# Kernel optimization log

Hardware: AMD Instinct MI355X
Metric: run time of the kernel (lower is better)

The kernel has to match this reference:

```python
import jax, jax.numpy as jnp
import numpy as np

N, E, C, FIN, FOUT = 4096, 5, 2, 128, 64
DENSITY = 0.01


def setup_inputs() -> dict:
    key = jax.random.key(0)
    ks = jax.random.split(key, 8)
    vals = jax.random.uniform(ks[0], (E, N, N), dtype=jnp.float32)
    mask = jax.random.uniform(ks[1], (E, N, N)) < DENSITY
    A = jnp.where(mask, vals, 0.0)                      # [E,N,N] edge-type adjacencies (A[e,u,v]: u->v)
    h = jax.random.normal(ks[2], (N, FIN), dtype=jnp.float32)
    W1_0 = 0.01 * jax.random.normal(ks[3], (C, E), dtype=jnp.float32)  # GTConv init: normal(std=0.01)
    W2_0 = 0.01 * jax.random.normal(ks[4], (C, E), dtype=jnp.float32)
    W1_1 = 0.01 * jax.random.normal(ks[5], (C, E), dtype=jnp.float32)
    gcn_W = jax.random.normal(ks[6], (C, FIN, FOUT), dtype=jnp.float32) / np.sqrt(FIN)
    gcn_b = jnp.zeros((C, FOUT), dtype=jnp.float32)
    return {"A": A, "h": h, "W1_0": W1_0, "W2_0": W2_0, "W1_1": W1_1,
            "gcn_W": gcn_W, "gcn_b": gcn_b}


def reference(A, h, W1_0, W2_0, W1_1, gcn_W, gcn_b):
    # Structural support of the summed graphs (union of edge-type edges).
    mask = (A != 0).any(axis=0)                         # [N,N]

    def gtconv(filt):
        # weighted sum of edge-type adjacencies per channel: dgl.adj_sum_graph
        return jnp.einsum('ce,euv->cuv', filt, A)       # [C,N,N]

    def right_norm(M, sum_axis):
        # EdgeWeightNorm(norm='right'): divide each edge weight by total in-weight at dst
        d = M.sum(axis=sum_axis, keepdims=True)
        return M / jnp.where(d != 0, d, 1.0)

    def softmax_norm(S):
        # exp on existing edges only, then right-normalize over in-edges (src axis=1)
        w = jnp.where(mask, jnp.exp(S), 0.0)
        return right_norm(w, sum_axis=1)

    # Layer 0 (first=True)
    RA = softmax_norm(gtconv(W1_0))                     # first_adj, [C,N,N]
    RB = softmax_norm(gtconv(W2_0))
    H0 = jnp.einsum('cuk,ckv->cuv', RA, RB)             # dgl.adj_product_graph
    # Layer 1 (first=False): result_A = H0, result_B = conv1(A) (no softmax)
    RB1 = gtconv(W1_1)
    H1 = jnp.einsum('cuk,ckv->cuv', H0, RB1)

    layers = jnp.stack([RA, H0, H1], axis=1)            # [C,3,N,N] = layer_list per channel
    Wn = right_norm(layers, sum_axis=2)                 # right norm over src (axis u)
    # GraphConv(norm='none', activation=relu) with edge_weight: out[v] = relu(sum_u w[u,v] h[u] W + b)
    agg = jnp.einsum('cluv,uf->clvf', Wn, h)            # [C,3,N,FIN]
    out = jax.nn.relu(jnp.einsum('clvf,cfo->clvo', agg, gcn_W) + gcn_b[:, None, None, :])
    return out                                          # [C,3,N,FOUT]
```

## Files before the change

### kernel.cpp

```cpp
#include <hip/hip_runtime.h>
#include <hip/hip_bf16.h>

#define NN    4096
#define NE    5
#define NC    2
#define FINF  128
#define FOUTF 64
#define CAP   384
#define YP    132
#define VB    16


__global__ __launch_bounds__(256) void zero_cnt(int4* __restrict__ cnt4)
{
    cnt4[blockIdx.x * 256 + threadIdx.x] = int4{0, 0, 0, 0};
}

__global__ __launch_bounds__(256) void build_csc(
    const float* __restrict__ A,
    const float* __restrict__ W1_0,
    const float* __restrict__ W2_0,
    const float* __restrict__ W1_1,
    int*    __restrict__ cnt,
    int*    __restrict__ eu,
    float2* __restrict__ wA,
    float2* __restrict__ wB,
    float2* __restrict__ wC)
{
    float fA0[NE], fA1[NE], fB0[NE], fB1[NE], fC0[NE], fC1[NE];
#pragma unroll
    for (int e = 0; e < NE; ++e) {
        fA0[e] = W1_0[e];      fA1[e] = W1_0[NE + e];
        fB0[e] = W2_0[e];      fB1[e] = W2_0[NE + e];
        fC0[e] = W1_1[e];      fC1[e] = W1_1[NE + e];
    }

    const size_t S = (size_t)NN * NN / 4;
    const float4* A4 = (const float4*)A;
    size_t stride = (size_t)gridDim.x * blockDim.x;
    for (size_t i = (size_t)blockIdx.x * blockDim.x + threadIdx.x; i < S; i += stride) {
        float4 q0 = A4[i];
        float4 q1 = A4[i + S];
        float4 q2 = A4[i + 2 * S];
        float4 q3 = A4[i + 3 * S];
        float4 q4 = A4[i + 4 * S];
        int u  = (int)(i >> 10);
        int v0 = ((int)i & 1023) << 2;
#define DO_COMP(comp, joff)                                                      \
        {                                                                        \
            float a0 = q0.comp, a1 = q1.comp, a2 = q2.comp,                      \
                  a3 = q3.comp, a4 = q4.comp;                                    \
            if (a0 != 0.f || a1 != 0.f || a2 != 0.f || a3 != 0.f || a4 != 0.f) { \
                float sA0 = fA0[0]*a0 + fA0[1]*a1 + fA0[2]*a2 + fA0[3]*a3 + fA0[4]*a4; \
                float sA1 = fA1[0]*a0 + fA1[1]*a1 + fA1[2]*a2 + fA1[3]*a3 + fA1[4]*a4; \
                float sB0 = fB0[0]*a0 + fB0[1]*a1 + fB0[2]*a2 + fB0[3]*a3 + fB0[4]*a4; \
                float sB1 = fB1[0]*a0 + fB1[1]*a1 + fB1[2]*a2 + fB1[3]*a3 + fB1[4]*a4; \
                float sC0 = fC0[0]*a0 + fC0[1]*a1 + fC0[2]*a2 + fC0[3]*a3 + fC0[4]*a4; \
                float sC1 = fC1[0]*a0 + fC1[1]*a1 + fC1[2]*a2 + fC1[3]*a3 + fC1[4]*a4; \
                int v = v0 + joff;                                               \
                int pos = atomicAdd(&cnt[v], 1);                                 \
                if (pos < CAP) {                                                 \
                    int slot = v * CAP + pos;                                    \
                    eu[slot] = u;                                                \
                    wA[slot] = float2{__expf(sA0), __expf(sA1)};                 \
                    wB[slot] = float2{__expf(sB0), __expf(sB1)};                 \
                    wC[slot] = float2{sC0, sC1};                                 \
                }                                                                \
            }                                                                    \
        }
        DO_COMP(x, 0)
        DO_COMP(y, 1)
        DO_COMP(z, 2)
        DO_COMP(w, 3)
#undef DO_COMP
    }
}

template<int STAGE>
__global__ __launch_bounds__(256) void spmm_col(
    const int*    __restrict__ cnt,
    const int*    __restrict__ eu,
    const float2* __restrict__ ew,
    const float*  __restrict__ Xf,
    const ushort* __restrict__ Xb_in,
    const float*  __restrict__ Dd_in,
    float*        __restrict__ Y,
    ushort*       __restrict__ Xb_out,
    float*        __restrict__ Dd_out)
{
    int v = blockIdx.x;
    int n = cnt[v];
    if (n > CAP) n = CAP;

    __shared__ float4 s_e[CAP];
    __shared__ float  s_red[4];
    __shared__ float4 s_acc[NC][8][32];

    int tid = threadIdx.x;
    if (tid < 4) s_red[tid] = 0.f;
    __syncthreads();

    float l0 = 0.f, l1 = 0.f, ld0 = 0.f, ld1 = 0.f;
    for (int i = tid; i < n; i += 256) {
        int    u = eu[v * CAP + i];
        float2 w = ew[v * CAP + i];
        s_e[i] = float4{__int_as_float(u), w.x, w.y, 0.f};
        l0 += w.x;
        l1 += w.y;
        if (STAGE != 0) {
            ld0 += w.x * Dd_in[u];
            ld1 += w.y * Dd_in[NN + u];
        }
    }
    if (STAGE == 0) { ld0 = l0; ld1 = l1; }

#pragma unroll
    for (int m = 32; m >= 1; m >>= 1) {
        l0  += __shfl_xor(l0,  m);
        l1  += __shfl_xor(l1,  m);
        ld0 += __shfl_xor(ld0, m);
        ld1 += __shfl_xor(ld1, m);
    }
    if ((tid & 63) == 0) {
        atomicAdd(&s_red[0], l0);
        atomicAdd(&s_red[1], l1);
        atomicAdd(&s_red[2], ld0);
        atomicAdd(&s_red[3], ld1);
    }
    __syncthreads();

    int grp = tid >> 5, lane = tid & 31;
    float4 a0 = {0.f, 0.f, 0.f, 0.f};
    float4 a1 = {0.f, 0.f, 0.f, 0.f};

    if (STAGE == 0) {
        const float4* X4 = (const float4*)Xf;
        for (int i = grp; i < n; i += 8) {
            float4 e = s_e[i];
            float4 x = X4[(size_t)__float_as_int(e.x) * 32 + lane];
            a0.x += e.y * x.x; a0.y += e.y * x.y; a0.z += e.y * x.z; a0.w += e.y * x.w;
            a1.x += e.z * x.x; a1.y += e.z * x.y; a1.z += e.z * x.z; a1.w += e.z * x.w;
        }
    } else {
        const uint2* P0 = (const uint2*)Xb_in;
        const uint2* P1 = P0 + (size_t)NN * 32;
        for (int i = grp; i < n; i += 8) {
            float4 e = s_e[i];
            int u = __float_as_int(e.x);
            uint2 b0 = P0[(size_t)u * 32 + lane];
            uint2 b1 = P1[(size_t)u * 32 + lane];
            a0.x += e.y * __uint_as_float(b0.x << 16);
            a0.y += e.y * __uint_as_float(b0.x & 0xffff0000u);
            a0.z += e.y * __uint_as_float(b0.y << 16);
            a0.w += e.y * __uint_as_float(b0.y & 0xffff0000u);
            a1.x += e.z * __uint_as_float(b1.x << 16);
            a1.y += e.z * __uint_as_float(b1.x & 0xffff0000u);
            a1.z += e.z * __uint_as_float(b1.y << 16);
            a1.w += e.z * __uint_as_float(b1.y & 0xffff0000u);
        }
    }

    s_acc[0][grp][lane] = a0;
    s_acc[1][grp][lane] = a1;
    __syncthreads();

    int c = tid >> 7, f = tid & 127;
    const float* base = (const float*)s_acc[c];
    float s = 0.f;
#pragma unroll
    for (int g = 0; g < 8; ++g) s += base[g * 128 + f];

    float inv = 1.f;
    if (STAGE < 2 && n > 0) inv = 1.f / s_red[c];
    float val = s * inv;

    float* yrow = Y + ((size_t)c * NN + v) * YP;
    yrow[f] = val;
    if (STAGE < 2) {
        __hip_bfloat16 hb = __float2bfloat16(val);
        Xb_out[((size_t)c * NN + v) * FINF + f] = *(const ushort*)&hb;
    }
    if (f == 0) {
        float dvn = s_red[2 + c] * inv;
        yrow[FINF] = dvn;
        if (STAGE < 2) Dd_out[c * NN + v] = dvn;
    }
}

__global__ __launch_bounds__(64) void gcn_out(
    const float* __restrict__ YA,
    const float* __restrict__ Y1,
    const float* __restrict__ Y2,
    const float* __restrict__ gW,
    const float* __restrict__ gb,
    float* __restrict__ out)
{
    const int grids_per_cl = NN / VB;
    int b   = blockIdx.x;
    int grp = b / grids_per_cl;
    int v0  = (b % grids_per_cl) * VB;
    int c = grp / 3, l = grp % 3;
    const float* Y = (l == 0) ? YA : (l == 1) ? Y1 : Y2;

    __shared__ float s_y[VB][FINF];
    __shared__ float s_inv[VB];
    int t = threadIdx.x;

    for (int k = t; k < VB * (FINF / 4); k += 64) {
        int r = k >> 5, c4 = k & 31;
        float4 q = *(const float4*)(Y + ((size_t)c * NN + v0 + r) * YP + c4 * 4);
        *(float4*)&s_y[r][c4 * 4] = q;
    }
    if (t < VB) {
        float d = Y[((size_t)c * NN + v0 + t) * YP + FINF];
        s_inv[t] = (d != 0.f) ? (1.f / d) : 1.f;
    }
    __syncthreads();

    float acc[VB];
#pragma unroll
    for (int r = 0; r < VB; ++r) acc[r] = 0.f;

    const float* w = gW + (size_t)c * FINF * FOUTF + t;
    for (int f4 = 0; f4 < FINF / 4; ++f4) {
        float w0 = w[(size_t)(f4 * 4 + 0) * FOUTF];
        float w1 = w[(size_t)(f4 * 4 + 1) * FOUTF];
        float w2 = w[(size_t)(f4 * 4 + 2) * FOUTF];
        float w3 = w[(size_t)(f4 * 4 + 3) * FOUTF];
#pragma unroll
        for (int r = 0; r < VB; ++r) {
            float4 y4 = *(const float4*)&s_y[r][f4 * 4];
            acc[r] += y4.x * w0 + y4.y * w1 + y4.z * w2 + y4.w * w3;
        }
    }

    float bias = gb[c * FOUTF + t];
#pragma unroll
    for (int r = 0; r < VB; ++r) {
        float val = acc[r] * s_inv[r] + bias;
        out[((size_t)grp * NN + v0 + r) * FOUTF + t] = fmaxf(val, 0.f);
    }
}

extern "C" void kernel_launch(void* const* d_in, const int* in_sizes, int n_in,
                              void* d_out, int out_size, void* d_ws, size_t ws_size,
                              hipStream_t stream)
{
    const float* A     = (const float*)d_in[0];
    const float* h     = (const float*)d_in[1];
    const float* W1_0  = (const float*)d_in[2];
    const float* W2_0  = (const float*)d_in[3];
    const float* W1_1  = (const float*)d_in[4];
    const float* gW    = (const float*)d_in[5];
    const float* gb    = (const float*)d_in[6];
    float* out = (float*)d_out;

    char* ws = (char*)d_ws;
    int*    cnt = (int*)(ws);
    int*    eu  = (int*)(ws + 16384);
    float2* wA  = (float2*)(ws + 6307840);
    float2* wB  = (float2*)(ws + 18890752);
    float2* wC  = (float2*)(ws + 31473664);
    float*  YA  = (float*)(ws + 44056576);
    float*  Y1  = (float*)(ws + 48381952);
    float*  Y2  = (float*)(ws + 52707328);
    float*  DdA = (float*)(ws + 57032704);
    float*  Dd1 = (float*)(ws + 57065472);
    ushort* XbA = (ushort*)(ws + 57098240);
    ushort* Xb1 = (ushort*)(ws + 59195392);

    zero_cnt<<<4, 256, 0, stream>>>((int4*)cnt);
    build_csc<<<2048, 256, 0, stream>>>(A, W1_0, W2_0, W1_1, cnt, eu, wA, wB, wC);

    spmm_col<0><<<NN, 256, 0, stream>>>(cnt, eu, wA, h, nullptr, nullptr, YA, XbA, DdA);
    spmm_col<1><<<NN, 256, 0, stream>>>(cnt, eu, wB, nullptr, XbA, DdA, Y1, Xb1, Dd1);
    spmm_col<2><<<NN, 256, 0, stream>>>(cnt, eu, wC, nullptr, Xb1, Dd1, Y2, nullptr, nullptr);

    gcn_out<<<6 * NN / VB, 64, 0, stream>>>(YA, Y1, Y2, gW, gb, out);
}
```

Measured before the change: 227.3 us.

## Tile CSC build by column block with LDS counters and bf16 feature input

The CSC build now gives each block a 16-column by 1024-row tile of A. Per-column counts are kept in shared-memory atomics and written into per-segment slots, which removes the global atomic contention and the separate zero-count kernel. The sparse aggregation reads the four segment counts and compacts them into shared memory. The first-stage input h is converted to bf16 by a new small kernel, which halves its gather traffic at some cost in precision. The gather loops are also unrolled by two. The tiled reads of A are less sequential than the old grid-stride stream, and the per-segment cap can drop edges if a quarter-column holds more than 128 nonzeros.

```diff
diff --git a/kernel.cpp b/kernel.cpp
--- a/kernel.cpp
+++ b/kernel.cpp
@@ -1,19 +1,33 @@
 #include <hip/hip_runtime.h>
 #include <hip/hip_bf16.h>
 
-#define NN    4096
-#define NE    5
-#define NC    2
-#define FINF  128
-#define FOUTF 64
-#define CAP   384
-#define YP    132
-#define VB    16
-
-
-__global__ __launch_bounds__(256) void zero_cnt(int4* __restrict__ cnt4)
-{
-    cnt4[blockIdx.x * 256 + threadIdx.x] = int4{0, 0, 0, 0};
+#define NN     4096
+#define NE     5
+#define NC     2
+#define FINF   128
+#define FOUTF  64
+#define CAP    512
+#define SEGCAP 128
+#define USPLIT 4
+#define YP     132
+#define VB     16
+
+
+static __device__ __forceinline__ unsigned bf16bits(float x)
+{
+    __hip_bfloat16 t = __float2bfloat16(x);
+    return (unsigned)*reinterpret_cast<unsigned short*>(&t);
+}
+
+__global__ __launch_bounds__(256) void h2b(const float4* __restrict__ h4,
+                                           uint2* __restrict__ hb)
+{
+    int i = blockIdx.x * 256 + threadIdx.x;
+    float4 f = h4[i];
+    uint2 r;
+    r.x = bf16bits(f.x) | (bf16bits(f.y) << 16);
+    r.y = bf16bits(f.z) | (bf16bits(f.w) << 16);
+    hb[i] = r;
 }
 
 __global__ __launch_bounds__(256) void build_csc(
@@ -21,12 +35,22 @@
     const float* __restrict__ W1_0,
     const float* __restrict__ W2_0,
     const float* __restrict__ W1_1,
-    int*    __restrict__ cnt,
+    int*    __restrict__ cnt2,
     int*    __restrict__ eu,
     float2* __restrict__ wA,
     float2* __restrict__ wB,
     float2* __restrict__ wC)
 {
+    __shared__ int lcnt[16];
+    int tid = threadIdx.x;
+    if (tid < 16) lcnt[tid] = 0;
+    __syncthreads();
+
+    int vb = blockIdx.x & 255;
+    int us = blockIdx.x >> 8;
+    int vbase = vb * 16;
+    int u0 = us * (NN / USPLIT);
+
     float fA0[NE], fA1[NE], fB0[NE], fB1[NE], fC0[NE], fC1[NE];
 #pragma unroll
     for (int e = 0; e < NE; ++e) {
@@ -35,18 +59,18 @@
         fC0[e] = W1_1[e];      fC1[e] = W1_1[NE + e];
     }
 
-    const size_t S = (size_t)NN * NN / 4;
-    const float4* A4 = (const float4*)A;
-    size_t stride = (size_t)gridDim.x * blockDim.x;
-    for (size_t i = (size_t)blockIdx.x * blockDim.x + threadIdx.x; i < S; i += stride) {
-        float4 q0 = A4[i];
-        float4 q1 = A4[i + S];
-        float4 q2 = A4[i + 2 * S];
-        float4 q3 = A4[i + 3 * S];
-        float4 q4 = A4[i + 4 * S];
-        int u  = (int)(i >> 10);
-        int v0 = ((int)i & 1023) << 2;
-#define DO_COMP(comp, joff)                                                      \
+    const size_t SL = (size_t)NN * NN;
+    int du = tid >> 2, dv4 = tid & 3;
+
+    for (int chunk = 0; chunk < (NN / USPLIT) / 64; ++chunk) {
+        int u = u0 + chunk * 64 + du;
+        const float* base = A + (size_t)u * NN + vbase + dv4 * 4;
+        float4 q0 = *(const float4*)(base);
+        float4 q1 = *(const float4*)(base + SL);
+        float4 q2 = *(const float4*)(base + 2 * SL);
+        float4 q3 = *(const float4*)(base + 3 * SL);
+        float4 q4 = *(const float4*)(base + 4 * SL);
+#define DO_COMP(comp, j)                                                         \
         {                                                                        \
             float a0 = q0.comp, a1 = q1.comp, a2 = q2.comp,                      \
                   a3 = q3.comp, a4 = q4.comp;                                    \
@@ -57,10 +81,10 @@
                 float sB1 = fB1[0]*a0 + fB1[1]*a1 + fB1[2]*a2 + fB1[3]*a3 + fB1[4]*a4; \
                 float sC0 = fC0[0]*a0 + fC0[1]*a1 + fC0[2]*a2 + fC0[3]*a3 + fC0[4]*a4; \
                 float sC1 = fC1[0]*a0 + fC1[1]*a1 + fC1[2]*a2 + fC1[3]*a3 + fC1[4]*a4; \
-                int v = v0 + joff;                                               \
-                int pos = atomicAdd(&cnt[v], 1);                                 \
-                if (pos < CAP) {                                                 \
-                    int slot = v * CAP + pos;                                    \
+                int lc = dv4 * 4 + j;                                            \
+                int pos = atomicAdd(&lcnt[lc], 1);               \
+                if (pos < SEGCAP) {                                              \
+                    int slot = (vbase + lc) * CAP + us * SEGCAP + pos;           \
                     eu[slot] = u;                                                \
                     wA[slot] = float2{__expf(sA0), __expf(sA1)};                 \
                     wB[slot] = float2{__expf(sB0), __expf(sB1)};                 \
@@ -74,23 +98,31 @@
         DO_COMP(w, 3)
 #undef DO_COMP
     }
+    __syncthreads();
+    if (tid < 16) {
+        int c = lcnt[tid];
+        cnt2[(vbase + tid) * USPLIT + us] = c < SEGCAP ? c : SEGCAP;
+    }
 }
 
 template<int STAGE>
 __global__ __launch_bounds__(256) void spmm_col(
-    const int*    __restrict__ cnt,
+    const int*    __restrict__ cnt2,
     const int*    __restrict__ eu,
     const float2* __restrict__ ew,
-    const float*  __restrict__ Xf,
-    const ushort* __restrict__ Xb_in,
+    const uint2*  __restrict__ Xb_in,
     const float*  __restrict__ Dd_in,
     float*        __restrict__ Y,
     ushort*       __restrict__ Xb_out,
     float*        __restrict__ Dd_out)
 {
     int v = blockIdx.x;
-    int n = cnt[v];
-    if (n > CAP) n = CAP;
+    int ns0 = cnt2[v * USPLIT + 0];
+    int ns1 = cnt2[v * USPLIT + 1];
+    int ns2 = cnt2[v * USPLIT + 2];
+    int ns3 = cnt2[v * USPLIT + 3];
+    int sb1 = ns0, sb2 = ns0 + ns1, sb3 = sb2 + ns2;
+    int n = sb3 + ns3;
 
     __shared__ float4 s_e[CAP];
     __shared__ float  s_red[4];
@@ -101,15 +133,21 @@
     __syncthreads();
 
     float l0 = 0.f, l1 = 0.f, ld0 = 0.f, ld1 = 0.f;
-    for (int i = tid; i < n; i += 256) {
-        int    u = eu[v * CAP + i];
-        float2 w = ew[v * CAP + i];
-        s_e[i] = float4{__int_as_float(u), w.x, w.y, 0.f};
-        l0 += w.x;
-        l1 += w.y;
-        if (STAGE != 0) {
-            ld0 += w.x * Dd_in[u];
-            ld1 += w.y * Dd_in[NN + u];
+#pragma unroll
+    for (int s = 0; s < USPLIT; ++s) {
+        int ns    = (s == 0) ? ns0 : (s == 1) ? ns1 : (s == 2) ? ns2 : ns3;
+        int sbase = (s == 0) ? 0   : (s == 1) ? sb1 : (s == 2) ? sb2 : sb3;
+        int gbase = v * CAP + s * SEGCAP;
+        for (int i = tid; i < ns; i += 256) {
+            int    u = eu[gbase + i];
+            float2 w = ew[gbase + i];
+            s_e[sbase + i] = float4{__int_as_float(u), w.x, w.y, 0.f};
+            l0 += w.x;
+            l1 += w.y;
+            if (STAGE != 0) {
+                ld0 += w.x * Dd_in[u];
+                ld1 += w.y * Dd_in[NN + u];
+            }
         }
     }
     if (STAGE == 0) { ld0 = l0; ld1 = l1; }
@@ -134,16 +172,21 @@
     float4 a1 = {0.f, 0.f, 0.f, 0.f};
 
     if (STAGE == 0) {
-        const float4* X4 = (const float4*)Xf;
+#pragma unroll 2
         for (int i = grp; i < n; i += 8) {
             float4 e = s_e[i];
-            float4 x = X4[(size_t)__float_as_int(e.x) * 32 + lane];
-            a0.x += e.y * x.x; a0.y += e.y * x.y; a0.z += e.y * x.z; a0.w += e.y * x.w;
-            a1.x += e.z * x.x; a1.y += e.z * x.y; a1.z += e.z * x.z; a1.w += e.z * x.w;
+            uint2 b = Xb_in[(size_t)__float_as_int(e.x) * 32 + lane];
+            float x0 = __uint_as_float(b.x << 16);
+            float x1 = __uint_as_float(b.x & 0xffff0000u);
+            float x2 = __uint_as_float(b.y << 16);
+            float x3 = __uint_as_float(b.y & 0xffff0000u);
+            a0.x += e.y * x0; a0.y += e.y * x1; a0.z += e.y * x2; a0.w += e.y * x3;
+            a1.x += e.z * x0; a1.y += e.z * x1; a1.z += e.z * x2; a1.w += e.z * x3;
         }
     } else {
-        const uint2* P0 = (const uint2*)Xb_in;
-        const uint2* P1 = P0 + (size_t)NN * 32;
+        const uint2* P0 = Xb_in;
+        const uint2* P1 = Xb_in + (size_t)NN * 32;
+#pragma unroll 2
         for (int i = grp; i < n; i += 8) {
             float4 e = s_e[i];
             int u = __float_as_int(e.x);
@@ -176,10 +219,8 @@
 
     float* yrow = Y + ((size_t)c * NN + v) * YP;
     yrow[f] = val;
-    if (STAGE < 2) {
-        __hip_bfloat16 hb = __float2bfloat16(val);
-        Xb_out[((size_t)c * NN + v) * FINF + f] = *(const ushort*)&hb;
-    }
+    if (STAGE < 2)
+        Xb_out[((size_t)c * NN + v) * FINF + f] = (ushort)bf16bits(val);
     if (f == 0) {
         float dvn = s_red[2 + c] * inv;
         yrow[FINF] = dvn;
@@ -256,25 +297,26 @@
     float* out = (float*)d_out;
 
     char* ws = (char*)d_ws;
-    int*    cnt = (int*)(ws);
-    int*    eu  = (int*)(ws + 16384);
-    float2* wA  = (float2*)(ws + 6307840);
-    float2* wB  = (float2*)(ws + 18890752);
-    float2* wC  = (float2*)(ws + 31473664);
-    float*  YA  = (float*)(ws + 44056576);
-    float*  Y1  = (float*)(ws + 48381952);
-    float*  Y2  = (float*)(ws + 52707328);
-    float*  DdA = (float*)(ws + 57032704);
-    float*  Dd1 = (float*)(ws + 57065472);
-    ushort* XbA = (ushort*)(ws + 57098240);
-    ushort* Xb1 = (ushort*)(ws + 59195392);
-
-    zero_cnt<<<4, 256, 0, stream>>>((int4*)cnt);
-    build_csc<<<2048, 256, 0, stream>>>(A, W1_0, W2_0, W1_1, cnt, eu, wA, wB, wC);
-
-    spmm_col<0><<<NN, 256, 0, stream>>>(cnt, eu, wA, h, nullptr, nullptr, YA, XbA, DdA);
-    spmm_col<1><<<NN, 256, 0, stream>>>(cnt, eu, wB, nullptr, XbA, DdA, Y1, Xb1, Dd1);
-    spmm_col<2><<<NN, 256, 0, stream>>>(cnt, eu, wC, nullptr, Xb1, Dd1, Y2, nullptr, nullptr);
+    int*    cnt2 = (int*)(ws);
+    int*    eu   = (int*)(ws + 65536);
+    float2* wA   = (float2*)(ws + 8454144);
+    float2* wB   = (float2*)(ws + 25231360);
+    float2* wC   = (float2*)(ws + 42008576);
+    float*  YA   = (float*)(ws + 58785792);
+    float*  Y1   = (float*)(ws + 63111168);
+    float*  Y2   = (float*)(ws + 67436544);
+    float*  DdA  = (float*)(ws + 71761920);
+    float*  Dd1  = (float*)(ws + 71794688);
+    uint2*  hb   = (uint2*)(ws + 71827456);
+    ushort* XbA  = (ushort*)(ws + 72876032);
+    ushort* Xb1  = (ushort*)(ws + 74973184);
+
+    h2b<<<512, 256, 0, stream>>>((const float4*)h, hb);
+    build_csc<<<256 * USPLIT, 256, 0, stream>>>(A, W1_0, W2_0, W1_1, cnt2, eu, wA, wB, wC);
+
+    spmm_col<0><<<NN, 256, 0, stream>>>(cnt2, eu, wA, hb, nullptr, YA, XbA, DdA);
+    spmm_col<1><<<NN, 256, 0, stream>>>(cnt2, eu, wB, (const uint2*)XbA, DdA, Y1, Xb1, Dd1);
+    spmm_col<2><<<NN, 256, 0, stream>>>(cnt2, eu, wC, (const uint2*)Xb1, Dd1, Y2, nullptr, nullptr);
 
     gcn_out<<<6 * NN / VB, 64, 0, stream>>>(YA, Y1, Y2, gW, gb, out);
 }
```

New measurement: 248.3 us. +9.3%, slower.

## Fuse GCN output projection into SpMM stages and gather bf16 h

Applied to the files above, without the earlier changes.

Removes the separate gcn_out kernel and the Y intermediate buffers by computing the 128x64 projection, bias and ReLU at the end of each spmm_col block for its node. h is pre-converted to bf16 inside a merged init kernel (which also zeros the counters), so stage 0 gathers half the bytes. The gather loops are also unrolled by 2. In exchange, each block re-reads gW with a per-thread serial 128-long dot product on only half the threads, and stage 0 now uses reduced-precision inputs.

```diff
diff --git a/kernel.cpp b/kernel.cpp
--- a/kernel.cpp
+++ b/kernel.cpp
@@ -7,13 +7,29 @@
 #define FINF  128
 #define FOUTF 64
 #define CAP   384
-#define YP    132
-#define VB    16
-
-
-__global__ __launch_bounds__(256) void zero_cnt(int4* __restrict__ cnt4)
-{
-    cnt4[blockIdx.x * 256 + threadIdx.x] = int4{0, 0, 0, 0};
+
+
+static __device__ __forceinline__ unsigned bf16bits(float x)
+{
+    __hip_bfloat16 t = __float2bfloat16(x);
+    return (unsigned)*reinterpret_cast<unsigned short*>(&t);
+}
+
+__global__ __launch_bounds__(256) void init_misc(int4* __restrict__ cnt4,
+                                                 const float4* __restrict__ h4,
+                                                 uint2* __restrict__ hb)
+{
+    int b = blockIdx.x;
+    if (b < 4) {
+        cnt4[b * 256 + threadIdx.x] = int4{0, 0, 0, 0};
+    } else {
+        int i = (b - 4) * 256 + threadIdx.x;
+        float4 f = h4[i];
+        uint2 r;
+        r.x = bf16bits(f.x) | (bf16bits(f.y) << 16);
+        r.y = bf16bits(f.z) | (bf16bits(f.w) << 16);
+        hb[i] = r;
+    }
 }
 
 __global__ __launch_bounds__(256) void build_csc(
@@ -81,10 +97,11 @@
     const int*    __restrict__ cnt,
     const int*    __restrict__ eu,
     const float2* __restrict__ ew,
-    const float*  __restrict__ Xf,
-    const ushort* __restrict__ Xb_in,
+    const uint2*  __restrict__ Xb_in,
     const float*  __restrict__ Dd_in,
-    float*        __restrict__ Y,
+    const float*  __restrict__ gW,
+    const float*  __restrict__ gb,
+    float*        __restrict__ out,
     ushort*       __restrict__ Xb_out,
     float*        __restrict__ Dd_out)
 {
@@ -95,6 +112,8 @@
     __shared__ float4 s_e[CAP];
     __shared__ float  s_red[4];
     __shared__ float4 s_acc[NC][8][32];
+    __shared__ float  s_y[NC][FINF];
+    __shared__ float  s_inv[NC];
 
     int tid = threadIdx.x;
     if (tid < 4) s_red[tid] = 0.f;
@@ -134,16 +153,21 @@
     float4 a1 = {0.f, 0.f, 0.f, 0.f};
 
     if (STAGE == 0) {
-        const float4* X4 = (const float4*)Xf;
+#pragma unroll 2
         for (int i = grp; i < n; i += 8) {
             float4 e = s_e[i];
-            float4 x = X4[(size_t)__float_as_int(e.x) * 32 + lane];
-            a0.x += e.y * x.x; a0.y += e.y * x.y; a0.z += e.y * x.z; a0.w += e.y * x.w;
-            a1.x += e.z * x.x; a1.y += e.z * x.y; a1.z += e.z * x.z; a1.w += e.z * x.w;
+            uint2 b = Xb_in[(size_t)__float_as_int(e.x) * 32 + lane];
+            float x0 = __uint_as_float(b.x << 16);
+            float x1 = __uint_as_float(b.x & 0xffff0000u);
+            float x2 = __uint_as_float(b.y << 16);
+            float x3 = __uint_as_float(b.y & 0xffff0000u);
+            a0.x += e.y * x0; a0.y += e.y * x1; a0.z += e.y * x2; a0.w += e.y * x3;
+            a1.x += e.z * x0; a1.y += e.z * x1; a1.z += e.z * x2; a1.w += e.z * x3;
         }
     } else {
-        const uint2* P0 = (const uint2*)Xb_in;
-        const uint2* P1 = P0 + (size_t)NN * 32;
+        const uint2* P0 = Xb_in;
+        const uint2* P1 = Xb_in + (size_t)NN * 32;
+#pragma unroll 2
         for (int i = grp; i < n; i += 8) {
             float4 e = s_e[i];
             int u = __float_as_int(e.x);
@@ -165,80 +189,37 @@
     __syncthreads();
 
     int c = tid >> 7, f = tid & 127;
-    const float* base = (const float*)s_acc[c];
-    float s = 0.f;
+    {
+        const float* base = (const float*)s_acc[c];
+        float s = 0.f;
 #pragma unroll
-    for (int g = 0; g < 8; ++g) s += base[g * 128 + f];
-
-    float inv = 1.f;
-    if (STAGE < 2 && n > 0) inv = 1.f / s_red[c];
-    float val = s * inv;
-
-    float* yrow = Y + ((size_t)c * NN + v) * YP;
-    yrow[f] = val;
-    if (STAGE < 2) {
-        __hip_bfloat16 hb = __float2bfloat16(val);
-        Xb_out[((size_t)c * NN + v) * FINF + f] = *(const ushort*)&hb;
-    }
-    if (f == 0) {
-        float dvn = s_red[2 + c] * inv;
-        yrow[FINF] = dvn;
-        if (STAGE < 2) Dd_out[c * NN + v] = dvn;
-    }
-}
-
-__global__ __launch_bounds__(64) void gcn_out(
-    const float* __restrict__ YA,
-    const float* __restrict__ Y1,
-    const float* __restrict__ Y2,
-    const float* __restrict__ gW,
-    const float* __restrict__ gb,
-    float* __restrict__ out)
-{
-    const int grids_per_cl = NN / VB;
-    int b   = blockIdx.x;
-    int grp = b / grids_per_cl;
-    int v0  = (b % grids_per_cl) * VB;
-    int c = grp / 3, l = grp % 3;
-    const float* Y = (l == 0) ? YA : (l == 1) ? Y1 : Y2;
-
-    __shared__ float s_y[VB][FINF];
-    __shared__ float s_inv[VB];
-    int t = threadIdx.x;
-
-    for (int k = t; k < VB * (FINF / 4); k += 64) {
-        int r = k >> 5, c4 = k & 31;
-        float4 q = *(const float4*)(Y + ((size_t)c * NN + v0 + r) * YP + c4 * 4);
-        *(float4*)&s_y[r][c4 * 4] = q;
-    }
-    if (t < VB) {
-        float d = Y[((size_t)c * NN + v0 + t) * YP + FINF];
-        s_inv[t] = (d != 0.f) ? (1.f / d) : 1.f;
-    }
-    __syncthreads();
-
-    float acc[VB];
-#pragma unroll
-    for (int r = 0; r < VB; ++r) acc[r] = 0.f;
-
-    const float* w = gW + (size_t)c * FINF * FOUTF + t;
-    for (int f4 = 0; f4 < FINF / 4; ++f4) {
-        float w0 = w[(size_t)(f4 * 4 + 0) * FOUTF];
-        float w1 = w[(size_t)(f4 * 4 + 1) * FOUTF];
-        float w2 = w[(size_t)(f4 * 4 + 2) * FOUTF];
-        float w3 = w[(size_t)(f4 * 4 + 3) * FOUTF];
-#pragma unroll
-        for (int r = 0; r < VB; ++r) {
-            float4 y4 = *(const float4*)&s_y[r][f4 * 4];
-            acc[r] += y4.x * w0 + y4.y * w1 + y4.z * w2 + y4.w * w3;
-        }
-    }
-
-    float bias = gb[c * FOUTF + t];
-#pragma unroll
-    for (int r = 0; r < VB; ++r) {
-        float val = acc[r] * s_inv[r] + bias;
-        out[((size_t)grp * NN + v0 + r) * FOUTF + t] = fmaxf(val, 0.f);
+        for (int g = 0; g < 8; ++g) s += base[g * 128 + f];
+
+        float inv = 1.f;
+        if (STAGE < 2 && n > 0) inv = 1.f / s_red[c];
+        float val = s * inv;
+
+        s_y[c][f] = val;
+        if (STAGE < 2)
+            Xb_out[((size_t)c * NN + v) * FINF + f] = (ushort)bf16bits(val);
+        if (f == 0) {
+            float dvn = s_red[2 + c] * inv;
+            s_inv[c] = (dvn != 0.f) ? (1.f / dvn) : 1.f;
+            if (STAGE < 2) Dd_out[c * NN + v] = dvn;
+        }
+    }
+    __syncthreads();
+
+    if (tid < 2 * FOUTF) {
+        int c2 = tid >> 6, o = tid & 63;
+        const float* w = gW + (size_t)c2 * FINF * FOUTF + o;
+        const float* y = s_y[c2];
+        float acc = 0.f;
+#pragma unroll 8
+        for (int f2 = 0; f2 < FINF; ++f2)
+            acc += y[f2] * w[(size_t)f2 * FOUTF];
+        float r = acc * s_inv[c2] + gb[c2 * FOUTF + o];
+        out[(((size_t)c2 * 3 + STAGE) * NN + v) * FOUTF + o] = fmaxf(r, 0.f);
     }
 }
 
@@ -261,20 +242,16 @@
     float2* wA  = (float2*)(ws + 6307840);
     float2* wB  = (float2*)(ws + 18890752);
     float2* wC  = (float2*)(ws + 31473664);
-    float*  YA  = (float*)(ws + 44056576);
-    float*  Y1  = (float*)(ws + 48381952);
-    float*  Y2  = (float*)(ws + 52707328);
-    float*  DdA = (float*)(ws + 57032704);
-    float*  Dd1 = (float*)(ws + 57065472);
-    ushort* XbA = (ushort*)(ws + 57098240);
-    ushort* Xb1 = (ushort*)(ws + 59195392);
-
-    zero_cnt<<<4, 256, 0, stream>>>((int4*)cnt);
+    float*  DdA = (float*)(ws + 44056576);
+    float*  Dd1 = (float*)(ws + 44089344);
+    uint2*  hb  = (uint2*)(ws + 44122112);
+    ushort* XbA = (ushort*)(ws + 45170688);
+    ushort* Xb1 = (ushort*)(ws + 47267840);
+
+    init_misc<<<516, 256, 0, stream>>>((int4*)cnt, (const float4*)h, hb);
     build_csc<<<2048, 256, 0, stream>>>(A, W1_0, W2_0, W1_1, cnt, eu, wA, wB, wC);
 
-    spmm_col<0><<<NN, 256, 0, stream>>>(cnt, eu, wA, h, nullptr, nullptr, YA, XbA, DdA);
-    spmm_col<1><<<NN, 256, 0, stream>>>(cnt, eu, wB, nullptr, XbA, DdA, Y1, Xb1, Dd1);
-    spmm_col<2><<<NN, 256, 0, stream>>>(cnt, eu, wC, nullptr, Xb1, Dd1, Y2, nullptr, nullptr);
-
-    gcn_out<<<6 * NN / VB, 64, 0, stream>>>(YA, Y1, Y2, gW, gb, out);
-}
+    spmm_col<0><<<NN, 256, 0, stream>>>(cnt, eu, wA, hb, nullptr, gW, gb, out, XbA, DdA);
+    spmm_col<1><<<NN, 256, 0, stream>>>(cnt, eu, wB, (const uint2*)XbA, DdA, gW, gb, out, Xb1, Dd1);
+    spmm_col<2><<<NN, 256, 0, stream>>>(cnt, eu, wC, (const uint2*)Xb1, Dd1, gW, gb, out, nullptr, nullptr);
+}
```

New measurement: 224.5 us. About the same (-1.2%).
